# Optimization experiments

Hardware: AMD Instinct MI355X
Metric: run time of the kernel (lower is better)

Reference implementation:

```python
import jax, jax.numpy as jnp
import numpy as np
from jax import lax

B, H, W = 16, 400, 400
NUM_PALETTE = 16

def _conv(x, w, b, stride, pad):
    y = lax.conv_general_dilated(x, w, (stride, stride), [(pad, pad), (pad, pad)],
                                 dimension_numbers=('NCHW', 'OIHW', 'NCHW'))
    return y + b[None, :, None, None]

def _leaky(x):
    return jnp.where(x >= 0, x, 0.01 * x)

def _palette(x, w1, b1, w2, b2, w3, b3, w4, b4, w5, b5, w6, b6):
    h = _leaky(_conv(x, w1, b1, 2, 1))   # [B,6,200,200]
    h = _leaky(_conv(h, w2, b2, 2, 1))   # [B,12,100,100]
    h = _leaky(_conv(h, w3, b3, 2, 1))   # [B,12,50,50]
    h = _leaky(_conv(h, w4, b4, 2, 1))   # [B,12,25,25]
    h = _leaky(_conv(h, w5, b5, 2, 1))   # [B,6,13,13]
    h = jax.nn.relu(_conv(h, w6, b6, 1, 0))  # [B,3,13,13]
    return h

def setup_inputs() -> dict:
    key = jax.random.key(0)
    ks = jax.random.split(key, 14)
    def he(k, shape):
        fan_in = shape[1] * shape[2] * shape[3]
        return jax.random.normal(k, shape, jnp.float32) * np.float32(np.sqrt(2.0 / fan_in))
    return {
        'x': jax.random.normal(ks[0], (B, 3, H, W), jnp.float32),
        'b_logits': jax.random.normal(ks[1], (B, NUM_PALETTE, H, W), jnp.float32),
        'w1': he(ks[2], (6, 3, 3, 3)),   'b1': jnp.zeros((6,), jnp.float32),
        'w2': he(ks[3], (12, 6, 3, 3)),  'b2': jnp.zeros((12,), jnp.float32),
        'w3': he(ks[4], (12, 12, 3, 3)), 'b3': jnp.zeros((12,), jnp.float32),
        'w4': he(ks[5], (12, 12, 3, 3)), 'b4': jnp.zeros((12,), jnp.float32),
        'w5': he(ks[6], (6, 12, 3, 3)),  'b5': jnp.zeros((6,), jnp.float32),
        'w6': he(ks[7], (3, 6, 1, 1)),   'b6': jnp.zeros((3,), jnp.float32),
    }

def reference(x, b_logits, w1, b1, w2, b2, w3, b3, w4, b4, w5, b5, w6, b6):
    # palette branch -> [B,3,13,13]; top-left 4x4 holds the 16 palette colors
    c = _palette(x, w1, b1, w2, b2, w3, b3, w4, b4, w5, b5, w6, b6)
    pal = c[:, :, :4, :4].reshape(c.shape[0], 3, NUM_PALETTE)  # [B,3,16], k = row*4+col
    # softmax over palette classes, one-hot of argmax via max-equality (ties kept, as in torch)
    probs = jax.nn.softmax(b_logits, axis=1)                    # [B,16,H,W]
    mx = jnp.max(probs, axis=1, keepdims=True)
    onehot = (probs == mx).astype(x.dtype)                      # [B,16,H,W]
    # per-pixel palette gather expressed as a contraction over the 16 classes
    result = jnp.einsum('bkhw,bck->bchw', onehot, pal)          # [B,3,H,W]
    return result
```

## Files before the change

kernel.cpp:

```cpp
#include <hip/hip_runtime.h>

#define HW 160000
#define WIMG 400

__global__ __launch_bounds__(256) void conv1_k(const float* __restrict__ x,
                                               const float* __restrict__ w,
                                               const float* __restrict__ bias,
                                               float* __restrict__ out) {
  int idx = blockIdx.x * 256 + threadIdx.x;
  int j = idx & 63;
  int i = (idx >> 6) & 63;
  int t = idx >> 12;
  int o = t % 6;
  int b = t / 6;
  float acc = bias[o];
#pragma unroll
  for (int c = 0; c < 3; c++) {
    const float* xc = x + (size_t)(b * 3 + c) * HW;
    const float* wc = w + (o * 3 + c) * 9;
#pragma unroll
    for (int di = 0; di < 3; di++) {
      int xi = 2 * i - 1 + di;
      if (xi < 0) continue;
#pragma unroll
      for (int dj = 0; dj < 3; dj++) {
        int xj = 2 * j - 1 + dj;
        if (xj < 0) continue;
        acc = fmaf(xc[xi * WIMG + xj], wc[di * 3 + dj], acc);
      }
    }
  }
  out[idx] = acc >= 0.f ? acc : 0.01f * acc;
}

__global__ __launch_bounds__(256) void conv2_k(const float* __restrict__ in,
                                               const float* __restrict__ w,
                                               const float* __restrict__ bias,
                                               float* __restrict__ out) {
  int idx = blockIdx.x * 256 + threadIdx.x;
  int j = idx & 31;
  int i = (idx >> 5) & 31;
  int t = idx >> 10;
  int o = t % 12;
  int b = t / 12;
  float acc = bias[o];
#pragma unroll
  for (int c = 0; c < 6; c++) {
    const float* xc = in + (size_t)(b * 6 + c) * 4096;
    const float* wc = w + (o * 6 + c) * 9;
#pragma unroll
    for (int di = 0; di < 3; di++) {
      int xi = 2 * i - 1 + di;
      if (xi < 0) continue;
#pragma unroll
      for (int dj = 0; dj < 3; dj++) {
        int xj = 2 * j - 1 + dj;
        if (xj < 0) continue;
        acc = fmaf(xc[xi * 64 + xj], wc[di * 3 + dj], acc);
      }
    }
  }
  out[idx] = acc >= 0.f ? acc : 0.01f * acc;
}

__global__ __launch_bounds__(256) void conv3456_k(
    const float* __restrict__ c2, const float* __restrict__ w3,
    const float* __restrict__ b3, const float* __restrict__ w4,
    const float* __restrict__ b4, const float* __restrict__ w5,
    const float* __restrict__ b5, const float* __restrict__ w6,
    const float* __restrict__ b6, float* __restrict__ pal) {
  __shared__ float s[12288];
  __shared__ float o3[3072];
  int tid = threadIdx.x;
  int b = blockIdx.x;

  for (int t = tid; t < 12288; t += 256) s[t] = c2[(size_t)b * 12288 + t];
  __syncthreads();

#pragma unroll
  for (int r = 0; r < 12; r++) {
    int idx = tid + 256 * r;
    int j = idx & 15, i = (idx >> 4) & 15, o = idx >> 8;
    float a = b3[o];
    for (int c = 0; c < 12; c++) {
      const float* wc = w3 + (o * 12 + c) * 9;
      const float* sc = s + c * 1024;
#pragma unroll
      for (int di = 0; di < 3; di++) {
        int xi = 2 * i - 1 + di;
        if (xi < 0) continue;
#pragma unroll
        for (int dj = 0; dj < 3; dj++) {
          int xj = 2 * j - 1 + dj;
          if (xj < 0) continue;
          a = fmaf(sc[xi * 32 + xj], wc[di * 3 + dj], a);
        }
      }
    }
    o3[idx] = a >= 0.f ? a : 0.01f * a;
  }
  __syncthreads();

#pragma unroll
  for (int r = 0; r < 3; r++) {
    int idx = tid + 256 * r;
    int j = idx & 7, i = (idx >> 3) & 7, o = idx >> 6;
    float a = b4[o];
    for (int c = 0; c < 12; c++) {
      const float* wc = w4 + (o * 12 + c) * 9;
      const float* sc = o3 + c * 256;
#pragma unroll
      for (int di = 0; di < 3; di++) {
        int xi = 2 * i - 1 + di;
        if (xi < 0) continue;
#pragma unroll
        for (int dj = 0; dj < 3; dj++) {
          int xj = 2 * j - 1 + dj;
          if (xj < 0) continue;
          a = fmaf(sc[xi * 16 + xj], wc[di * 3 + dj], a);
        }
      }
    }
    __syncthreads();
    s[idx] = a >= 0.f ? a : 0.01f * a;
  }
  __syncthreads();

  if (tid < 96) {
    int j = tid & 3, i = (tid >> 2) & 3, o = tid >> 4;
    float a = b5[o];
    for (int c = 0; c < 12; c++) {
      const float* wc = w5 + (o * 12 + c) * 9;
      const float* sc = s + c * 64;
#pragma unroll
      for (int di = 0; di < 3; di++) {
        int xi = 2 * i - 1 + di;
        if (xi < 0) continue;
#pragma unroll
        for (int dj = 0; dj < 3; dj++) {
          int xj = 2 * j - 1 + dj;
          if (xj < 0) continue;
          a = fmaf(sc[xi * 8 + xj], wc[di * 3 + dj], a);
        }
      }
    }
    s[1024 + tid] = a >= 0.f ? a : 0.01f * a;
  }
  __syncthreads();

  if (tid < 48) {
    int k = tid & 15, o = tid >> 4;
    float a = b6[o];
#pragma unroll
    for (int c = 0; c < 6; c++) a = fmaf(s[1024 + c * 16 + k], w6[o * 6 + c], a);
    pal[b * 48 + o * 16 + k] = a > 0.f ? a : 0.f;
  }
}

__global__ __launch_bounds__(256) void gather_k(const float* __restrict__ logits,
                                                const float* __restrict__ pal,
                                                float* __restrict__ out) {
  __shared__ float ps[48];
  int b = blockIdx.y;
  int tid = threadIdx.x;
  if (tid < 48) ps[tid] = pal[b * 48 + tid];
  __syncthreads();
  int q = blockIdx.x * 256 + tid;
  if (q >= HW / 4) return;
  const float* lg = logits + (size_t)b * 16 * HW + q * 4;

  float4 t[16];
#pragma unroll
  for (int k = 0; k < 16; k++) t[k] = *(const float4*)(lg + (size_t)k * HW);

  float mx[4] = {t[0].x, t[0].y, t[0].z, t[0].w};
  float p0 = ps[0], p1 = ps[16], p2 = ps[32];
  float r0[4] = {p0, p0, p0, p0};
  float r1[4] = {p1, p1, p1, p1};
  float r2[4] = {p2, p2, p2, p2};

#pragma unroll
  for (int k = 1; k < 16; k++) {
    float q0 = ps[k], q1 = ps[16 + k], q2 = ps[32 + k];
    float vv[4] = {t[k].x, t[k].y, t[k].z, t[k].w};
#pragma unroll
    for (int pp = 0; pp < 4; pp++) {
      float val = vv[pp];
      bool gt = val > mx[pp];
      bool ge = val >= mx[pp];
      mx[pp] = ge ? val : mx[pp];
      r0[pp] = (gt ? 0.f : r0[pp]) + (ge ? q0 : 0.f);
      r1[pp] = (gt ? 0.f : r1[pp]) + (ge ? q1 : 0.f);
      r2[pp] = (gt ? 0.f : r2[pp]) + (ge ? q2 : 0.f);
    }
  }
  float* ob = out + (size_t)b * 3 * HW + q * 4;
  *(float4*)(ob) = make_float4(r0[0], r0[1], r0[2], r0[3]);
  *(float4*)(ob + HW) = make_float4(r1[0], r1[1], r1[2], r1[3]);
  *(float4*)(ob + 2 * HW) = make_float4(r2[0], r2[1], r2[2], r2[3]);
}

extern "C" void kernel_launch(void* const* d_in, const int* in_sizes, int n_in,
                              void* d_out, int out_size, void* d_ws, size_t ws_size,
                              hipStream_t stream) {
  const float* x    = (const float*)d_in[0];
  const float* blog = (const float*)d_in[1];
  const float* w1 = (const float*)d_in[2];
  const float* b1 = (const float*)d_in[3];
  const float* w2 = (const float*)d_in[4];
  const float* b2 = (const float*)d_in[5];
  const float* w3 = (const float*)d_in[6];
  const float* b3 = (const float*)d_in[7];
  const float* w4 = (const float*)d_in[8];
  const float* b4 = (const float*)d_in[9];
  const float* w5 = (const float*)d_in[10];
  const float* b5 = (const float*)d_in[11];
  const float* w6 = (const float*)d_in[12];
  const float* b6 = (const float*)d_in[13];
  float* out = (float*)d_out;

  float* c1  = (float*)d_ws;
  float* c2  = c1 + 16 * 6 * 64 * 64;
  float* pal = c2 + 16 * 12 * 32 * 32;

  conv1_k<<<1536, 256, 0, stream>>>(x, w1, b1, c1);
  conv2_k<<<768, 256, 0, stream>>>(c1, w2, b2, c2);
  conv3456_k<<<16, 256, 0, stream>>>(c2, w3, b3, w4, b4, w5, b5, w6, b6, pal);
  gather_k<<<dim3((HW / 4 + 255) / 256, 16), 256, 0, stream>>>(blog, pal, out);
}
```

Before: 383.9 us.

## Split conv3 into its own wide-grid kernel and use nontemporal loads/stores in gather

Conv3 moves out of the 16-block fused tail kernel into a templated stride-2 conv kernel launched with 192 blocks, so it spreads across many more CUs instead of 16 blocks each doing 12 serial rounds from LDS. The remaining conv4-6 kernel reads conv3 output from global memory and uses much less shared memory. The gather kernel switches to nontemporal loads and stores for the streamed logits and output. In exchange there is one extra kernel launch and a global round trip for the conv3 activations.

```diff
diff --git a/kernel.cpp b/kernel.cpp
--- a/kernel.cpp
+++ b/kernel.cpp
@@ -2,6 +2,8 @@
 
 #define HW 160000
 #define WIMG 400
+
+typedef float v4 __attribute__((ext_vector_type(4)));
 
 __global__ __launch_bounds__(256) void conv1_k(const float* __restrict__ x,
                                                const float* __restrict__ w,
@@ -33,21 +35,23 @@
   out[idx] = acc >= 0.f ? acc : 0.01f * acc;
 }
 
-__global__ __launch_bounds__(256) void conv2_k(const float* __restrict__ in,
+template <int N, int CIN>
+__global__ __launch_bounds__(256) void convs_k(const float* __restrict__ in,
                                                const float* __restrict__ w,
                                                const float* __restrict__ bias,
-                                               float* __restrict__ out) {
+                                               float* __restrict__ out,
+                                               int cout) {
   int idx = blockIdx.x * 256 + threadIdx.x;
-  int j = idx & 31;
-  int i = (idx >> 5) & 31;
-  int t = idx >> 10;
-  int o = t % 12;
-  int b = t / 12;
+  int j = idx & (N - 1);
+  int i = (idx / N) & (N - 1);
+  int t = idx / (N * N);
+  int o = t % cout;
+  int b = t / cout;
   float acc = bias[o];
 #pragma unroll
-  for (int c = 0; c < 6; c++) {
-    const float* xc = in + (size_t)(b * 6 + c) * 4096;
-    const float* wc = w + (o * 6 + c) * 9;
+  for (int c = 0; c < CIN; c++) {
+    const float* xc = in + (size_t)(b * CIN + c) * (4 * N * N);
+    const float* wc = w + (o * CIN + c) * 9;
 #pragma unroll
     for (int di = 0; di < 3; di++) {
       int xi = 2 * i - 1 + di;
@@ -56,50 +60,23 @@
       for (int dj = 0; dj < 3; dj++) {
         int xj = 2 * j - 1 + dj;
         if (xj < 0) continue;
-        acc = fmaf(xc[xi * 64 + xj], wc[di * 3 + dj], acc);
+        acc = fmaf(xc[xi * 2 * N + xj], wc[di * 3 + dj], acc);
       }
     }
   }
   out[idx] = acc >= 0.f ? acc : 0.01f * acc;
 }
 
-__global__ __launch_bounds__(256) void conv3456_k(
-    const float* __restrict__ c2, const float* __restrict__ w3,
-    const float* __restrict__ b3, const float* __restrict__ w4,
+__global__ __launch_bounds__(256) void conv456_k(
+    const float* __restrict__ c3, const float* __restrict__ w4,
     const float* __restrict__ b4, const float* __restrict__ w5,
     const float* __restrict__ b5, const float* __restrict__ w6,
     const float* __restrict__ b6, float* __restrict__ pal) {
-  __shared__ float s[12288];
-  __shared__ float o3[3072];
+  __shared__ float s4[768];
+  __shared__ float s5[96];
   int tid = threadIdx.x;
   int b = blockIdx.x;
-
-  for (int t = tid; t < 12288; t += 256) s[t] = c2[(size_t)b * 12288 + t];
-  __syncthreads();
-
-#pragma unroll
-  for (int r = 0; r < 12; r++) {
-    int idx = tid + 256 * r;
-    int j = idx & 15, i = (idx >> 4) & 15, o = idx >> 8;
-    float a = b3[o];
-    for (int c = 0; c < 12; c++) {
-      const float* wc = w3 + (o * 12 + c) * 9;
-      const float* sc = s + c * 1024;
-#pragma unroll
-      for (int di = 0; di < 3; di++) {
-        int xi = 2 * i - 1 + di;
-        if (xi < 0) continue;
-#pragma unroll
-        for (int dj = 0; dj < 3; dj++) {
-          int xj = 2 * j - 1 + dj;
-          if (xj < 0) continue;
-          a = fmaf(sc[xi * 32 + xj], wc[di * 3 + dj], a);
-        }
-      }
-    }
-    o3[idx] = a >= 0.f ? a : 0.01f * a;
-  }
-  __syncthreads();
+  const float* cb = c3 + (size_t)b * 12 * 256;
 
 #pragma unroll
   for (int r = 0; r < 3; r++) {
@@ -108,7 +85,7 @@
     float a = b4[o];
     for (int c = 0; c < 12; c++) {
       const float* wc = w4 + (o * 12 + c) * 9;
-      const float* sc = o3 + c * 256;
+      const float* sc = cb + c * 256;
 #pragma unroll
       for (int di = 0; di < 3; di++) {
         int xi = 2 * i - 1 + di;
@@ -121,8 +98,7 @@
         }
       }
     }
-    __syncthreads();
-    s[idx] = a >= 0.f ? a : 0.01f * a;
+    s4[idx] = a >= 0.f ? a : 0.01f * a;
   }
   __syncthreads();
 
@@ -131,7 +107,7 @@
     float a = b5[o];
     for (int c = 0; c < 12; c++) {
       const float* wc = w5 + (o * 12 + c) * 9;
-      const float* sc = s + c * 64;
+      const float* sc = s4 + c * 64;
 #pragma unroll
       for (int di = 0; di < 3; di++) {
         int xi = 2 * i - 1 + di;
@@ -144,7 +120,7 @@
         }
       }
     }
-    s[1024 + tid] = a >= 0.f ? a : 0.01f * a;
+    s5[tid] = a >= 0.f ? a : 0.01f * a;
   }
   __syncthreads();
 
@@ -152,7 +128,7 @@
     int k = tid & 15, o = tid >> 4;
     float a = b6[o];
 #pragma unroll
-    for (int c = 0; c < 6; c++) a = fmaf(s[1024 + c * 16 + k], w6[o * 6 + c], a);
+    for (int c = 0; c < 6; c++) a = fmaf(s5[c * 16 + k], w6[o * 6 + c], a);
     pal[b * 48 + o * 16 + k] = a > 0.f ? a : 0.f;
   }
 }
@@ -169,9 +145,10 @@
   if (q >= HW / 4) return;
   const float* lg = logits + (size_t)b * 16 * HW + q * 4;
 
-  float4 t[16];
-#pragma unroll
-  for (int k = 0; k < 16; k++) t[k] = *(const float4*)(lg + (size_t)k * HW);
+  v4 t[16];
+#pragma unroll
+  for (int k = 0; k < 16; k++)
+    t[k] = __builtin_nontemporal_load((const v4*)(lg + (size_t)k * HW));
 
   float mx[4] = {t[0].x, t[0].y, t[0].z, t[0].w};
   float p0 = ps[0], p1 = ps[16], p2 = ps[32];
@@ -195,9 +172,12 @@
     }
   }
   float* ob = out + (size_t)b * 3 * HW + q * 4;
-  *(float4*)(ob) = make_float4(r0[0], r0[1], r0[2], r0[3]);
-  *(float4*)(ob + HW) = make_float4(r1[0], r1[1], r1[2], r1[3]);
-  *(float4*)(ob + 2 * HW) = make_float4(r2[0], r2[1], r2[2], r2[3]);
+  v4 s0 = {r0[0], r0[1], r0[2], r0[3]};
+  v4 s1 = {r1[0], r1[1], r1[2], r1[3]};
+  v4 s2 = {r2[0], r2[1], r2[2], r2[3]};
+  __builtin_nontemporal_store(s0, (v4*)ob);
+  __builtin_nontemporal_store(s1, (v4*)(ob + HW));
+  __builtin_nontemporal_store(s2, (v4*)(ob + 2 * HW));
 }
 
 extern "C" void kernel_launch(void* const* d_in, const int* in_sizes, int n_in,
@@ -221,10 +201,12 @@
 
   float* c1  = (float*)d_ws;
   float* c2  = c1 + 16 * 6 * 64 * 64;
-  float* pal = c2 + 16 * 12 * 32 * 32;
+  float* c3  = c2 + 16 * 12 * 32 * 32;
+  float* pal = c3 + 16 * 12 * 16 * 16;
 
   conv1_k<<<1536, 256, 0, stream>>>(x, w1, b1, c1);
-  conv2_k<<<768, 256, 0, stream>>>(c1, w2, b2, c2);
-  conv3456_k<<<16, 256, 0, stream>>>(c2, w3, b3, w4, b4, w5, b5, w6, b6, pal);
+  convs_k<32, 6><<<768, 256, 0, stream>>>(c1, w2, b2, c2, 12);
+  convs_k<16, 12><<<192, 256, 0, stream>>>(c2, w3, b3, c3, 12);
+  conv456_k<<<16, 256, 0, stream>>>(c3, w4, b4, w5, b5, w6, b6, pal);
   gather_k<<<dim3((HW / 4 + 255) / 256, 16), 256, 0, stream>>>(blog, pal, out);
 }
```

New measurement: 327.4 us. 1.17x faster.
